# Kernel tuning notes

Hardware: AMD Instinct MI355X
Metric: run time of the kernel (lower is better)

## Reference

```python
import jax, jax.numpy as jnp
import numpy as np

N = 50000      # nodes
E = 800000     # edges (avg degree 16)
H = 128        # hidden_dim
F_IN = 128     # node_in_dim
EPS = 1e-8     # torch cosine_similarity eps
ALPHA = 0.3


def _xavier(k, shape):
    fan_out, fan_in = shape
    lim = float(np.sqrt(6.0 / (fan_in + fan_out)))
    return jax.random.uniform(k, shape, minval=-lim, maxval=lim, dtype=jnp.float32)


PARAM_SHAPES = [
    ("w_lq", (H, 1)), ("w_lf", (H, F_IN)),
    ("wq0", (H, 1)), ("wq1", (H, H)), ("wq2", (H, H)),
    ("wx0", (H, F_IN)), ("wx1", (H, H)), ("wx2", (H, H)),
    ("wf0", (H, H)), ("wf1", (H, H)), ("wf2", (H, H)),
    ("m1_w1", (H, H)), ("m1_w2", (H, H)),
    ("m2_w1", (1, H)), ("m2_w2", (1, 1)),
]
BIAS_OF = {"w_lq": "b_lq", "w_lf": "b_lf", "wq0": "bq0", "wq1": "bq1", "wq2": "bq2",
           "wx0": "bx0", "wx1": "bx1", "wx2": "bx2", "wf0": "bf0", "wf1": "bf1",
           "wf2": "bf2", "m1_w1": "m1_b1", "m1_w2": "m1_b2", "m2_w1": "m2_b1", "m2_w2": "m2_b2"}


def setup_inputs() -> dict:
    key = jax.random.key(0)
    ks = jax.random.split(key, 3 + len(PARAM_SHAPES))
    inp = {
        "q": 42,
        "feats": jax.random.normal(ks[0], (N, F_IN), dtype=jnp.float32),
        "edge_index": jax.random.randint(ks[1], (2, E), 0, N, dtype=jnp.int64),
        "neg_edge_index": jax.random.randint(ks[2], (2, E), 0, N, dtype=jnp.int64),
    }
    for i, (name, shape) in enumerate(PARAM_SHAPES):
        inp[name] = _xavier(ks[3 + i], shape)
        inp[BIAS_OF[name]] = jnp.zeros((shape[0],), jnp.float32)
    return inp


def _forward(q, feats, edge_index, neg_edge_index,
             w_lq, b_lq, w_lf, b_lf,
             wq0, bq0, wq1, bq1, wq2, bq2,
             wx0, bx0, wx1, bx1, wx2, bx2,
             wf0, bf0, wf1, bf1, wf2, bf2,
             m1_w1, m1_b1, m1_w2, m1_b2,
             m2_w1, m2_b1, m2_w2, m2_b2):
    n = feats.shape[0]
    src, dst = edge_index[0], edge_index[1]

    # GCN symmetric normalization with self-loops (edge_weight = 1)
    deg = jax.ops.segment_sum(jnp.ones(src.shape[0], feats.dtype), dst, num_segments=n) + 1.0
    dis = deg ** -0.5
    norm_e = dis[src] * dis[dst]        # per-edge norm
    inv_deg = 1.0 / deg                 # self-loop norm d^-1/2 * d^-1/2

    def lin(x, W, b):
        return x @ W.T + b

    def gcn(x, W, b):
        xw = x @ W.T                                                      # [n,H]
        agg = jax.ops.segment_sum(xw[src] * norm_e[:, None], dst, num_segments=n)
        return agg + xw * inv_deg[:, None] + b

    querys = jnp.zeros((n, 1), feats.dtype).at[q, 0].set(1.0)
    querys_ = lin(querys, w_lq, b_lq)
    feats_ = lin(feats, w_lf, b_lf)

    # layer 0
    hq = jax.nn.relu(gcn(querys, wq0, bq0))
    h = jax.nn.relu(gcn(feats, wx0, bx0))
    hf = jax.nn.relu(hq + h + gcn(querys_ + feats_, wf0, bf0))
    # middle layer (num_layers - 2 == 1 iteration, eval mode: dropout identity)
    hq = jax.nn.relu(gcn(hq, wq1, bq1))
    h = jax.nn.relu(gcn(h, wx1, bx1))
    hf = jax.nn.relu(hq + h + gcn(hf, wf1, bf1))
    # final layer (no relu)
    hq = gcn(hq, wq2, bq2)
    h = gcn(h, wx2, bx2)
    hf = hq + h + gcn(hf, wf2, bf2)

    x = lin(jax.nn.relu(lin(hf, m1_w1, m1_b1)), m1_w2, m1_b2)  # mlp1

    # ---- decode (attack_type != 'proposed') ----
    q_emb = x[q]
    qn = jnp.maximum(jnp.linalg.norm(q_emb), EPS)

    def cos_q(v):  # cosine similarity of rows of v with q_emb (torch eps semantics)
        vn = jnp.maximum(jnp.linalg.norm(v, axis=-1), EPS)
        return (v @ q_emb) / (vn * qn)

    # reconstruct loss: BCE-with-logits on cosine edge scores
    pos_s = cos_q((x[src] + x[dst]) * 0.5)
    neg_s = cos_q((x[neg_edge_index[0]] + x[neg_edge_index[1]]) * 0.5)
    loss_recon = jnp.mean(jax.nn.softplus(-pos_s)) + jnp.mean(jax.nn.softplus(neg_s))

    sim_xq = cos_q(x)                                            # [n]
    sim_xx = lin(jax.nn.relu(lin(x, m2_w1, m2_b1)), m2_w2, m2_b2)[:, 0]  # mlp2
    sim = ((1.0 - ALPHA) * sim_xq + ALPHA * sim_xx) * 2.0
    return jax.nn.sigmoid(sim), loss_recon


def reference(q, feats, edge_index, neg_edge_index,
              w_lq, b_lq, w_lf, b_lf,
              wq0, bq0, wq1, bq1, wq2, bq2,
              wx0, bx0, wx1, bx1, wx2, bx2,
              wf0, bf0, wf1, bf1, wf2, bf2,
              m1_w1, m1_b1, m1_w2, m1_b2,
              m2_w1, m2_b1, m2_w2, m2_b2):
    return _forward(q, feats, edge_index, neg_edge_index,
                    w_lq, b_lq, w_lf, b_lf,
                    wq0, bq0, wq1, bq1, wq2, bq2,
                    wx0, bx0, wx1, bx1, wx2, bx2,
                    wf0, bf0, wf1, bf1, wf2, bf2,
                    m1_w1, m1_b1, m1_w2, m1_b2,
                    m2_w1, m2_b1, m2_w2, m2_b2)
```

## Files before the change

### kernel.cpp

```cpp
#include <hip/hip_runtime.h>
#include <math.h>

#define N_NODES 50000
#define N_EDGES 800000
#define EPSV 1e-8f
#define ALPHA 0.3f

typedef __attribute__((ext_vector_type(8))) unsigned short ushort8;
typedef __attribute__((ext_vector_type(8))) short short8;
typedef __attribute__((ext_vector_type(4))) float floatx4;

__device__ inline float b2f(unsigned short u) {
    union { unsigned i; float f; } c; c.i = ((unsigned)u) << 16; return c.f;
}
__device__ inline unsigned short f2b(float f) {
    union { float f; unsigned i; } c; c.f = f;
    return (unsigned short)((c.i + 0x7FFFu + ((c.i >> 16) & 1u)) >> 16);
}


__global__ __launch_bounds__(256) void k_count(const int* __restrict__ ei,
                                               int* __restrict__ cnt) {
    int e = blockIdx.x * 256 + threadIdx.x;
    if (e < N_EDGES) atomicAdd(&cnt[ei[N_EDGES + e]], 1);
}

__global__ __launch_bounds__(256) void k_invdis(const int* __restrict__ cnt,
                                                float* __restrict__ dis,
                                                float* __restrict__ inv) {
    int i = blockIdx.x * 256 + threadIdx.x;
    if (i < N_NODES) {
        float d = (float)cnt[i] + 1.0f;
        dis[i] = 1.0f / sqrtf(d);
        inv[i] = 1.0f / d;
    }
}

__global__ __launch_bounds__(256) void k_scan_partial(const int* __restrict__ cnt,
                                                      int* __restrict__ partial) {
    int b = blockIdx.x, t = threadIdx.x;
    int base = b * 1024 + t * 4;
    int s = 0;
#pragma unroll
    for (int j = 0; j < 4; ++j) {
        int idx = base + j;
        if (idx < N_NODES) s += cnt[idx];
    }
#pragma unroll
    for (int m = 1; m < 64; m <<= 1) s += __shfl_xor(s, m, 64);
    __shared__ int sh[4];
    if ((t & 63) == 0) sh[t >> 6] = s;
    __syncthreads();
    if (t == 0) partial[b] = sh[0] + sh[1] + sh[2] + sh[3];
}

__global__ void k_scan_mid(int* __restrict__ partial, int* __restrict__ rowptr) {
    int l = threadIdx.x;
    const int NP = (N_NODES + 1023) / 1024;
    int v = (l < NP) ? partial[l] : 0;
    int vin = v;
#pragma unroll
    for (int off = 1; off < 64; off <<= 1) {
        int u = __shfl_up(v, off, 64);
        if (l >= off) v += u;
    }
    if (l < NP) partial[l] = v - vin;
    if (l == NP - 1) rowptr[N_NODES] = v;
}

__global__ __launch_bounds__(256) void k_scan_final(const int* __restrict__ cnt,
                                                    const int* __restrict__ partial,
                                                    int* __restrict__ rowptr) {
    int b = blockIdx.x, t = threadIdx.x;
    int base = b * 1024 + t * 4;
    int c[4];
    int s = 0;
#pragma unroll
    for (int j = 0; j < 4; ++j) {
        int idx = base + j;
        c[j] = (idx < N_NODES) ? cnt[idx] : 0;
        s += c[j];
    }
    __shared__ int sh[256];
    sh[t] = s;
    __syncthreads();
    for (int off = 1; off < 256; off <<= 1) {
        int v = 0;
        if (t >= off) v = sh[t - off];
        __syncthreads();
        sh[t] += v;
        __syncthreads();
    }
    int texcl = sh[t] - s;
    int pre = partial[b] + texcl;
#pragma unroll
    for (int j = 0; j < 4; ++j) {
        int idx = base + j;
        if (idx < N_NODES) rowptr[idx] = pre;
        pre += c[j];
    }
}

__global__ __launch_bounds__(256) void k_fill(const int* __restrict__ ei,
                                              const int* __restrict__ rowptr,
                                              int* __restrict__ cursor,
                                              int* __restrict__ col) {
    int e = blockIdx.x * 256 + threadIdx.x;
    if (e < N_EDGES) {
        int d = ei[N_EDGES + e];
        int pos = rowptr[d] + atomicAdd(&cursor[d], 1);
        col[pos] = ei[e];
    }
}

__global__ __launch_bounds__(256) void k_t(const int* __restrict__ ei,
                                           const int* __restrict__ qp,
                                           const float* __restrict__ dis,
                                           const float* __restrict__ inv,
                                           float* __restrict__ t) {
    int e = blockIdx.x * 256 + threadIdx.x;
    int q = *qp;
    if (e == 0) atomicAdd(&t[q], inv[q]);
    if (e < N_EDGES && ei[e] == q) {
        int d = ei[N_EDGES + e];
        atomicAdd(&t[d], dis[q] * dis[d]);
    }
}

__global__ __launch_bounds__(256) void k_cast(const float* __restrict__ in,
                                              unsigned short* __restrict__ out, int n8) {
    int id = blockIdx.x * 256 + threadIdx.x;
    if (id >= n8) return;
    const float4 a = *(const float4*)(in + id * 8);
    const float4 b = *(const float4*)(in + id * 8 + 4);
    ushort8 o;
    o[0] = f2b(a.x); o[1] = f2b(a.y); o[2] = f2b(a.z); o[3] = f2b(a.w);
    o[4] = f2b(b.x); o[5] = f2b(b.y); o[6] = f2b(b.z); o[7] = f2b(b.w);
    *(ushort8*)(out + id * 8) = o;
}


template <int RELU, int NADD, int HASB2, int WF32>
__global__ __launch_bounds__(256) void k_gemm(
    const unsigned short* __restrict__ A, int As,
    const float* __restrict__ W,
    const float* __restrict__ bias, const float* __restrict__ bias2,
    const unsigned short* __restrict__ add1, int a1s,
    const unsigned short* __restrict__ add2, int a2s,
    unsigned short* __restrict__ outh, int ohs,
    float* __restrict__ outf, int ofs, int nrows) {
    __shared__ unsigned short Al[128 * 128];
    __shared__ unsigned short Wl[128 * 128];
    const int tid = threadIdx.x;
    const int row0 = blockIdx.x * 128;
    const int t4 = tid >> 4, c16 = tid & 15;

#pragma unroll
    for (int it = 0; it < 8; ++it) {
        int r = it * 16 + t4;
        int gr = row0 + r; if (gr > nrows - 1) gr = nrows - 1;
        ushort8 v = *(const ushort8*)(A + (size_t)gr * As + c16 * 8);
        int boff = (c16 * 16) ^ ((r & 7) << 4);
        *(ushort8*)((char*)Al + r * 256 + boff) = v;
    }
#pragma unroll
    for (int it = 0; it < 8; ++it) {
        int c = it * 16 + t4;
        const float* wp = W + c * 128 + c16 * 8;
        float4 w0 = *(const float4*)wp;
        float4 w1 = *(const float4*)(wp + 4);
        ushort8 v;
        v[0] = f2b(w0.x); v[1] = f2b(w0.y); v[2] = f2b(w0.z); v[3] = f2b(w0.w);
        v[4] = f2b(w1.x); v[5] = f2b(w1.y); v[6] = f2b(w1.z); v[7] = f2b(w1.w);
        int boff = (c16 * 16) ^ ((c & 7) << 4);
        *(ushort8*)((char*)Wl + c * 256 + boff) = v;
    }
    __syncthreads();

    const int wv = tid >> 6, l = tid & 63;
    const int lr = l & 15, lg = l >> 4;
    const int sx = (lr & 7) << 4;

    floatx4 acc[8][2];
#pragma unroll
    for (int i = 0; i < 8; ++i)
#pragma unroll
        for (int j = 0; j < 2; ++j) acc[i][j] = (floatx4){0.f, 0.f, 0.f, 0.f};

#pragma unroll
    for (int ks = 0; ks < 4; ++ks) {
        int ko = (ks * 64 + lg * 16) ^ sx;
        short8 bfr[2];
#pragma unroll
        for (int ct = 0; ct < 2; ++ct) {
            int c = wv * 32 + ct * 16 + lr;
            bfr[ct] = *(const short8*)((char*)Wl + c * 256 + ko);
        }
#pragma unroll
        for (int rt = 0; rt < 8; ++rt) {
            int r = rt * 16 + lr;
            short8 af = *(const short8*)((char*)Al + r * 256 + ko);
            acc[rt][0] = __builtin_amdgcn_mfma_f32_16x16x32_bf16(af, bfr[0], acc[rt][0], 0, 0, 0);
            acc[rt][1] = __builtin_amdgcn_mfma_f32_16x16x32_bf16(af, bfr[1], acc[rt][1], 0, 0, 0);
        }
    }

#pragma unroll
    for (int ct = 0; ct < 2; ++ct) {
        int colc = wv * 32 + ct * 16 + lr;
        float bv = bias[colc];
        if (HASB2) bv += bias2[colc];
#pragma unroll
        for (int rt = 0; rt < 8; ++rt) {
            int rbase = row0 + rt * 16 + lg * 4;
#pragma unroll
            for (int reg = 0; reg < 4; ++reg) {
                int r = rbase + reg;
                if (r >= nrows) continue;
                float v = acc[rt][ct][reg] + bv;
                if (NADD >= 1) v += b2f(add1[(size_t)r * a1s + colc]);
                if (NADD >= 2) v += b2f(add2[(size_t)r * a2s + colc]);
                if (RELU) v = fmaxf(v, 0.f);
                outh[(size_t)r * ohs + colc] = f2b(v);
                if (WF32) outf[(size_t)r * ofs + colc] = v;
            }
        }
    }
}


__global__ void k_agg(const int* __restrict__ rowptr, const int* __restrict__ col,
                      const float* __restrict__ dis, const float* __restrict__ inv,
                      const unsigned short* __restrict__ in, int ins, int incb,
                      unsigned short* __restrict__ out, int outs, int outcb) {
    int i = blockIdx.x;
    int cb = blockIdx.y * 128;
    int l = threadIdx.x;
    int g = l >> 4, li = l & 15;
    int r0 = rowptr[i], r1 = rowptr[i + 1];
    float acc[8] = {0.f, 0.f, 0.f, 0.f, 0.f, 0.f, 0.f, 0.f};
    for (int base = r0; base < r1; base += 4) {
        int e = base + g;
        float w = 0.f;
        int s = i;
        if (e < r1) { s = col[e]; w = dis[s]; }
        ushort8 v = *(const ushort8*)(in + (size_t)s * ins + incb + cb + li * 8);
#pragma unroll
        for (int j = 0; j < 8; ++j) acc[j] = fmaf(w, b2f(v[j]), acc[j]);
    }
#pragma unroll
    for (int j = 0; j < 8; ++j) {
        acc[j] += __shfl_xor(acc[j], 16, 64);
        acc[j] += __shfl_xor(acc[j], 32, 64);
    }
    if (g == 0) {
        ushort8 sv = *(const ushort8*)(in + (size_t)i * ins + incb + cb + li * 8);
        float di = dis[i], iv = inv[i];
        ushort8 o;
#pragma unroll
        for (int j = 0; j < 8; ++j) o[j] = f2b(fmaf(di, acc[j], iv * b2f(sv[j])));
        *(ushort8*)(out + (size_t)i * outs + outcb + cb + li * 8) = o;
    }
}

__global__ __launch_bounds__(256) void k_hq0(const float* __restrict__ t,
                                             const float* __restrict__ wq0,
                                             const float* __restrict__ bq0,
                                             unsigned short* __restrict__ B1h) {
    int gidx = blockIdx.x * 256 + threadIdx.x;
    int i = gidx >> 7, j = gidx & 127;
    B1h[(size_t)i * 384 + j] = f2b(fmaxf(fmaf(t[i], wq0[j], bq0[j]), 0.f));
}

__global__ void k_addwlq(const int* __restrict__ qp, const float* __restrict__ w_lq,
                         unsigned short* __restrict__ z0h) {
    int j = threadIdx.x;
    int q = *qp;
    z0h[(size_t)q * 128 + j] = f2b(b2f(z0h[(size_t)q * 128 + j]) + w_lq[j]);
}


__global__ void k_qemb(const int* __restrict__ qp, const float* __restrict__ xf,
                       float* __restrict__ qe) {
    int j = threadIdx.x;
    int q = *qp;
    float v = xf[(size_t)q * 128 + j];
    qe[j] = v;
    float s = v * v;
#pragma unroll
    for (int m = 1; m < 64; m <<= 1) s += __shfl_xor(s, m, 64);
    __shared__ float sh[2];
    if ((j & 63) == 0) sh[j >> 6] = s;
    __syncthreads();
    if (j == 0) qe[128] = fmaxf(sqrtf(sh[0] + sh[1]), EPSV);
}

__global__ __launch_bounds__(256) void k_node(const float* __restrict__ xf,
                                              const float* __restrict__ qe,
                                              const float* __restrict__ m2w1,
                                              const float* __restrict__ m2b1,
                                              const float* __restrict__ m2w2,
                                              const float* __restrict__ m2b2,
                                              float* __restrict__ out,
                                              float* __restrict__ a,
                                              float* __restrict__ n2) {
    int node = blockIdx.x * 4 + (threadIdx.x >> 6);
    int lane = threadIdx.x & 63;
    const float2 xv = *(const float2*)(xf + (size_t)node * 128 + 2 * lane);
    const float2 qv = *(const float2*)(qe + 2 * lane);
    const float2 wv = *(const float2*)(m2w1 + 2 * lane);
    float dq = xv.x * qv.x + xv.y * qv.y;
    float dx = xv.x * xv.x + xv.y * xv.y;
    float dw = xv.x * wv.x + xv.y * wv.y;
#pragma unroll
    for (int m = 1; m < 64; m <<= 1) {
        dq += __shfl_xor(dq, m, 64);
        dx += __shfl_xor(dx, m, 64);
        dw += __shfl_xor(dw, m, 64);
    }
    if (lane == 0) {
        float qn = qe[128];
        float vn = fmaxf(sqrtf(dx), EPSV);
        float simq = dq / (vn * qn);
        float l1 = dw + m2b1[0];
        float s2 = fmaxf(l1, 0.f) * m2w2[0] + m2b2[0];
        float sim = ((1.f - ALPHA) * simq + ALPHA * s2) * 2.f;
        out[node] = 1.f / (1.f + expf(-sim));
        a[node] = dq;
        n2[node] = dx;
    }
}

__global__ __launch_bounds__(256) void k_loss(const int* __restrict__ ei,
                                              const int* __restrict__ nei,
                                              const unsigned short* __restrict__ xh,
                                              const float* __restrict__ a,
                                              const float* __restrict__ n2,
                                              const float* __restrict__ qe,
                                              float* __restrict__ lossout) {
    int l = threadIdx.x & 63, wvi = threadIdx.x >> 6;
    int g = l >> 4, li = l & 15;
    float qn = qe[128];
    float local = 0.f;
    const int tot = 2 * N_EDGES;
    const int stride = gridDim.x * 16;
    for (int e = blockIdx.x * 16 + wvi * 4 + g; e < tot; e += stride) {
        const int* Ep = (e < N_EDGES) ? ei : nei;
        int eo = (e < N_EDGES) ? e : e - N_EDGES;
        int s = Ep[eo], d = Ep[eo + N_EDGES];
        ushort8 va = *(const ushort8*)(xh + (size_t)s * 128 + li * 8);
        ushort8 vb = *(const ushort8*)(xh + (size_t)d * 128 + li * 8);
        float dsd = 0.f;
#pragma unroll
        for (int j = 0; j < 8; ++j) dsd = fmaf(b2f(va[j]), b2f(vb[j]), dsd);
        dsd += __shfl_xor(dsd, 1, 64);
        dsd += __shfl_xor(dsd, 2, 64);
        dsd += __shfl_xor(dsd, 4, 64);
        dsd += __shfl_xor(dsd, 8, 64);
        if (li == 0) {
            float nv = 0.25f * (n2[s] + n2[d] + 2.f * dsd);
            float vn = fmaxf(sqrtf(fmaxf(nv, 0.f)), EPSV);
            float num = 0.5f * (a[s] + a[d]);
            float cs = num / (vn * qn);
            float sg = (e < N_EDGES) ? -cs : cs;
            local += log1pf(expf(sg));
        }
    }
    local += __shfl_xor(local, 16, 64);
    local += __shfl_xor(local, 32, 64);
    __shared__ float sh[4];
    if (l == 0) sh[wvi] = local;
    __syncthreads();
    if (threadIdx.x == 0)
        atomicAdd(lossout, (sh[0] + sh[1] + sh[2] + sh[3]) * (1.f / N_EDGES));
}


extern "C" void kernel_launch(void* const* d_in, const int* in_sizes, int n_in,
                              void* d_out, int out_size, void* d_ws, size_t ws_size,
                              hipStream_t stream) {
    const int* qp = (const int*)d_in[0];
    const float* feats = (const float*)d_in[1];
    const int* ei = (const int*)d_in[2];
    const int* nei = (const int*)d_in[3];
    const float *w_lq = (const float*)d_in[4], *b_lq = (const float*)d_in[5];
    const float *w_lf = (const float*)d_in[6], *b_lf = (const float*)d_in[7];
    const float *wq0 = (const float*)d_in[8], *bq0 = (const float*)d_in[9];
    const float *wq1 = (const float*)d_in[10], *bq1 = (const float*)d_in[11];
    const float *wq2 = (const float*)d_in[12], *bq2 = (const float*)d_in[13];
    const float *wx0 = (const float*)d_in[14], *bx0 = (const float*)d_in[15];
    const float *wx1 = (const float*)d_in[16], *bx1 = (const float*)d_in[17];
    const float *wx2 = (const float*)d_in[18], *bx2 = (const float*)d_in[19];
    const float *wf0 = (const float*)d_in[20], *bf0 = (const float*)d_in[21];
    const float *wf1 = (const float*)d_in[22], *bf1 = (const float*)d_in[23];
    const float *wf2 = (const float*)d_in[24], *bf2 = (const float*)d_in[25];
    const float *m1w1 = (const float*)d_in[26], *m1b1 = (const float*)d_in[27];
    const float *m1w2 = (const float*)d_in[28], *m1b2 = (const float*)d_in[29];
    const float *m2w1 = (const float*)d_in[30], *m2b1 = (const float*)d_in[31];
    const float *m2w2 = (const float*)d_in[32], *m2b2 = (const float*)d_in[33];
    float* out = (float*)d_out;

    char* p = (char*)d_ws;
    auto alloc = [&](size_t b) -> char* {
        char* r = p;
        p += (b + 255) & ~(size_t)255;
        return r;
    };
    float* dis = (float*)alloc(N_NODES * 4);
    float* inv = (float*)alloc(N_NODES * 4);
    float* t = (float*)alloc(N_NODES * 4);
    float* qe = (float*)alloc(129 * 4);
    float* a = (float*)alloc(N_NODES * 4);
    float* n2 = (float*)alloc(N_NODES * 4);
    int* cnt = (int*)alloc(N_NODES * 4);
    int* cursor = (int*)alloc(N_NODES * 4);
    int* rowptr = (int*)alloc((N_NODES + 1) * 4);
    int* partial = (int*)alloc(64 * 4);
    int* col = (int*)alloc(N_EDGES * 4);
    unsigned short* featsh = (unsigned short*)alloc((size_t)N_NODES * 128 * 2);
    unsigned short* z0h = (unsigned short*)alloc((size_t)N_NODES * 128 * 2);
    unsigned short* B1h = (unsigned short*)alloc((size_t)N_NODES * 384 * 2);
    unsigned short* B2h = (unsigned short*)alloc((size_t)N_NODES * 384 * 2);
    unsigned short* xh = (unsigned short*)alloc((size_t)N_NODES * 128 * 2);
    float* xf = (float*)alloc((size_t)N_NODES * 128 * 4);

    const int EB = (N_EDGES + 255) / 256;
    const int NB = (N_NODES + 255) / 256;
    const int NP = (N_NODES + 1023) / 1024;
    const int GB = (N_NODES + 127) / 128;

    hipMemsetAsync(cnt, 0, N_NODES * 4, stream);
    hipMemsetAsync(cursor, 0, N_NODES * 4, stream);
    hipMemsetAsync(t, 0, N_NODES * 4, stream);
    hipMemsetAsync(out + N_NODES, 0, 4, stream);

    k_count<<<EB, 256, 0, stream>>>(ei, cnt);
    k_invdis<<<NB, 256, 0, stream>>>(cnt, dis, inv);
    k_scan_partial<<<NP, 256, 0, stream>>>(cnt, partial);
    k_scan_mid<<<1, 64, 0, stream>>>(partial, rowptr);
    k_scan_final<<<NP, 256, 0, stream>>>(cnt, partial, rowptr);
    k_fill<<<EB, 256, 0, stream>>>(ei, rowptr, cursor, col);
    k_t<<<EB, 256, 0, stream>>>(ei, qp, dis, inv, t);
    k_cast<<<(N_NODES * 128 / 8 + 255) / 256, 256, 0, stream>>>(feats, featsh,
                                                                N_NODES * 128 / 8);

    k_gemm<0, 0, 1, 0><<<GB, 256, 0, stream>>>(featsh, 128, w_lf, b_lf, b_lq,
                                               nullptr, 0, nullptr, 0,
                                               z0h, 128, nullptr, 0, N_NODES);
    k_addwlq<<<1, 128, 0, stream>>>(qp, w_lq, z0h);

    k_hq0<<<(N_NODES * 128) / 256, 256, 0, stream>>>(t, wq0, bq0, B1h);
    k_agg<<<dim3(N_NODES, 1), 64, 0, stream>>>(rowptr, col, dis, inv, featsh, 128, 0,
                                               B2h, 384, 128);
    k_agg<<<dim3(N_NODES, 1), 64, 0, stream>>>(rowptr, col, dis, inv, z0h, 128, 0,
                                               B2h, 384, 256);
    k_gemm<1, 0, 0, 0><<<GB, 256, 0, stream>>>(B2h + 128, 384, wx0, bx0, nullptr,
                                               nullptr, 0, nullptr, 0,
                                               B1h + 128, 384, nullptr, 0, N_NODES);
    k_gemm<1, 2, 0, 0><<<GB, 256, 0, stream>>>(B2h + 256, 384, wf0, bf0, nullptr,
                                               B1h + 0, 384, B1h + 128, 384,
                                               B1h + 256, 384, nullptr, 0, N_NODES);

    k_agg<<<dim3(N_NODES, 3), 64, 0, stream>>>(rowptr, col, dis, inv, B1h, 384, 0,
                                               B2h, 384, 0);
    k_gemm<1, 0, 0, 0><<<GB, 256, 0, stream>>>(B2h + 0, 384, wq1, bq1, nullptr,
                                               nullptr, 0, nullptr, 0,
                                               B1h + 0, 384, nullptr, 0, N_NODES);
    k_gemm<1, 0, 0, 0><<<GB, 256, 0, stream>>>(B2h + 128, 384, wx1, bx1, nullptr,
                                               nullptr, 0, nullptr, 0,
                                               B1h + 128, 384, nullptr, 0, N_NODES);
    k_gemm<1, 2, 0, 0><<<GB, 256, 0, stream>>>(B2h + 256, 384, wf1, bf1, nullptr,
                                               B1h + 0, 384, B1h + 128, 384,
                                               B1h + 256, 384, nullptr, 0, N_NODES);

    k_agg<<<dim3(N_NODES, 3), 64, 0, stream>>>(rowptr, col, dis, inv, B1h, 384, 0,
                                               B2h, 384, 0);
    k_gemm<0, 0, 0, 0><<<GB, 256, 0, stream>>>(B2h + 0, 384, wq2, bq2, nullptr,
                                               nullptr, 0, nullptr, 0,
                                               B1h + 0, 384, nullptr, 0, N_NODES);
    k_gemm<0, 0, 0, 0><<<GB, 256, 0, stream>>>(B2h + 128, 384, wx2, bx2, nullptr,
                                               nullptr, 0, nullptr, 0,
                                               B1h + 128, 384, nullptr, 0, N_NODES);
    k_gemm<0, 2, 0, 0><<<GB, 256, 0, stream>>>(B2h + 256, 384, wf2, bf2, nullptr,
                                               B1h + 0, 384, B1h + 128, 384,
                                               B1h + 256, 384, nullptr, 0, N_NODES);

    k_gemm<1, 0, 0, 0><<<GB, 256, 0, stream>>>(B1h + 256, 384, m1w1, m1b1, nullptr,
                                               nullptr, 0, nullptr, 0,
                                               B2h + 0, 384, nullptr, 0, N_NODES);
    k_gemm<0, 0, 0, 1><<<GB, 256, 0, stream>>>(B2h + 0, 384, m1w2, m1b2, nullptr,
                                               nullptr, 0, nullptr, 0,
                                               xh, 128, xf, 128, N_NODES);

    k_qemb<<<1, 128, 0, stream>>>(qp, xf, qe);
    k_node<<<N_NODES / 4, 256, 0, stream>>>(xf, qe, m2w1, m2b1, m2w2, m2b2, out, a, n2);
    k_loss<<<4096, 256, 0, stream>>>(ei, nei, xh, a, n2, qe, out + N_NODES);
}
```

Baseline: 734.3 us.

## Pre-cast weights to bf16, load GEMM tiles via global_load_lds, batch agg rows, fp16 loss dot

All eleven 128x128 weight matrices are now converted to bf16 once by a single batched kernel, so GEMM blocks no longer convert fp32 weights per block. GEMM tiles for A and W are fetched with direct global-to-LDS loads that keep the swizzled layout. The aggregation kernel now packs four nodes per 256-thread block instead of one node per 64-thread block. The final x is stored as fp16 and the loss kernel uses packed fdot2 products, which changes numerics from bf16 to fp16 for that path.

Result: no change. 737.4 us (+0.4%).

```diff
diff --git a/kernel.cpp b/kernel.cpp
--- a/kernel.cpp
+++ b/kernel.cpp
@@ -9,6 +9,7 @@
 typedef __attribute__((ext_vector_type(8))) unsigned short ushort8;
 typedef __attribute__((ext_vector_type(8))) short short8;
 typedef __attribute__((ext_vector_type(4))) float floatx4;
+typedef _Float16 half2v __attribute__((ext_vector_type(2)));
 
 __device__ inline float b2f(unsigned short u) {
     union { unsigned i; float f; } c; c.i = ((unsigned)u) << 16; return c.f;
@@ -16,6 +17,9 @@
 __device__ inline unsigned short f2b(float f) {
     union { float f; unsigned i; } c; c.f = f;
     return (unsigned short)((c.i + 0x7FFFu + ((c.i >> 16) & 1u)) >> 16);
+}
+__device__ inline unsigned short f2h(float f) {
+    union { _Float16 h; unsigned short u; } c; c.h = (_Float16)f; return c.u;
 }
 
 
@@ -139,11 +143,24 @@
     *(ushort8*)(out + id * 8) = o;
 }
 
-
-template <int RELU, int NADD, int HASB2, int WF32>
+struct WPack { const float* w[11]; };
+__global__ __launch_bounds__(256) void k_castw(WPack wp, unsigned short* __restrict__ out) {
+    int m = blockIdx.y;
+    int id = blockIdx.x * 256 + threadIdx.x;
+    const float* src = wp.w[m] + id * 8;
+    float4 a = *(const float4*)src;
+    float4 b = *(const float4*)(src + 4);
+    ushort8 o;
+    o[0] = f2b(a.x); o[1] = f2b(a.y); o[2] = f2b(a.z); o[3] = f2b(a.w);
+    o[4] = f2b(b.x); o[5] = f2b(b.y); o[6] = f2b(b.z); o[7] = f2b(b.w);
+    *(ushort8*)(out + m * 16384 + id * 8) = o;
+}
+
+
+template <int RELU, int NADD, int HASB2, int WOUT>
 __global__ __launch_bounds__(256) void k_gemm(
     const unsigned short* __restrict__ A, int As,
-    const float* __restrict__ W,
+    const unsigned short* __restrict__ Wb,
     const float* __restrict__ bias, const float* __restrict__ bias2,
     const unsigned short* __restrict__ add1, int a1s,
     const unsigned short* __restrict__ add2, int a2s,
@@ -153,31 +170,28 @@
     __shared__ unsigned short Wl[128 * 128];
     const int tid = threadIdx.x;
     const int row0 = blockIdx.x * 128;
+    const int wv = tid >> 6;
     const int t4 = tid >> 4, c16 = tid & 15;
 
 #pragma unroll
     for (int it = 0; it < 8; ++it) {
         int r = it * 16 + t4;
         int gr = row0 + r; if (gr > nrows - 1) gr = nrows - 1;
-        ushort8 v = *(const ushort8*)(A + (size_t)gr * As + c16 * 8);
-        int boff = (c16 * 16) ^ ((r & 7) << 4);
-        *(ushort8*)((char*)Al + r * 256 + boff) = v;
-    }
-#pragma unroll
-    for (int it = 0; it < 8; ++it) {
-        int c = it * 16 + t4;
-        const float* wp = W + c * 128 + c16 * 8;
-        float4 w0 = *(const float4*)wp;
-        float4 w1 = *(const float4*)(wp + 4);
-        ushort8 v;
-        v[0] = f2b(w0.x); v[1] = f2b(w0.y); v[2] = f2b(w0.z); v[3] = f2b(w0.w);
-        v[4] = f2b(w1.x); v[5] = f2b(w1.y); v[6] = f2b(w1.z); v[7] = f2b(w1.w);
-        int boff = (c16 * 16) ^ ((c & 7) << 4);
-        *(ushort8*)((char*)Wl + c * 256 + boff) = v;
+        int sw = (c16 * 16) ^ ((r & 7) << 4);
+        const char* srcA = (const char*)(A + (size_t)gr * As) + sw;
+        __builtin_amdgcn_global_load_lds(
+            (const __attribute__((address_space(1))) void*)srcA,
+            (__attribute__((address_space(3))) void*)(Al + it * 2048 + wv * 512),
+            16, 0, 0);
+        const char* srcW = (const char*)(Wb + r * 128) + sw;
+        __builtin_amdgcn_global_load_lds(
+            (const __attribute__((address_space(1))) void*)srcW,
+            (__attribute__((address_space(3))) void*)(Wl + it * 2048 + wv * 512),
+            16, 0, 0);
     }
     __syncthreads();
 
-    const int wv = tid >> 6, l = tid & 63;
+    const int l = tid & 63;
     const int lr = l & 15, lg = l >> 4;
     const int sx = (lr & 7) << 4;
 
@@ -221,21 +235,26 @@
                 if (NADD >= 1) v += b2f(add1[(size_t)r * a1s + colc]);
                 if (NADD >= 2) v += b2f(add2[(size_t)r * a2s + colc]);
                 if (RELU) v = fmaxf(v, 0.f);
-                outh[(size_t)r * ohs + colc] = f2b(v);
-                if (WF32) outf[(size_t)r * ofs + colc] = v;
+                if (WOUT) {
+                    outh[(size_t)r * ohs + colc] = f2h(v);
+                    outf[(size_t)r * ofs + colc] = v;
+                } else {
+                    outh[(size_t)r * ohs + colc] = f2b(v);
+                }
             }
         }
     }
 }
 
 
-__global__ void k_agg(const int* __restrict__ rowptr, const int* __restrict__ col,
-                      const float* __restrict__ dis, const float* __restrict__ inv,
-                      const unsigned short* __restrict__ in, int ins, int incb,
-                      unsigned short* __restrict__ out, int outs, int outcb) {
-    int i = blockIdx.x;
+__global__ __launch_bounds__(256) void k_agg(
+    const int* __restrict__ rowptr, const int* __restrict__ col,
+    const float* __restrict__ dis, const float* __restrict__ inv,
+    const unsigned short* __restrict__ in, int ins,
+    unsigned short* __restrict__ out, int outs, int outcb) {
+    int i = blockIdx.x * 4 + (threadIdx.x >> 6);
     int cb = blockIdx.y * 128;
-    int l = threadIdx.x;
+    int l = threadIdx.x & 63;
     int g = l >> 4, li = l & 15;
     int r0 = rowptr[i], r1 = rowptr[i + 1];
     float acc[8] = {0.f, 0.f, 0.f, 0.f, 0.f, 0.f, 0.f, 0.f};
@@ -244,7 +263,7 @@
         float w = 0.f;
         int s = i;
         if (e < r1) { s = col[e]; w = dis[s]; }
-        ushort8 v = *(const ushort8*)(in + (size_t)s * ins + incb + cb + li * 8);
+        ushort8 v = *(const ushort8*)(in + (size_t)s * ins + cb + li * 8);
 #pragma unroll
         for (int j = 0; j < 8; ++j) acc[j] = fmaf(w, b2f(v[j]), acc[j]);
     }
@@ -254,7 +273,7 @@
         acc[j] += __shfl_xor(acc[j], 32, 64);
     }
     if (g == 0) {
-        ushort8 sv = *(const ushort8*)(in + (size_t)i * ins + incb + cb + li * 8);
+        ushort8 sv = *(const ushort8*)(in + (size_t)i * ins + cb + li * 8);
         float di = dis[i], iv = inv[i];
         ushort8 o;
 #pragma unroll
@@ -348,11 +367,13 @@
         const int* Ep = (e < N_EDGES) ? ei : nei;
         int eo = (e < N_EDGES) ? e : e - N_EDGES;
         int s = Ep[eo], d = Ep[eo + N_EDGES];
-        ushort8 va = *(const ushort8*)(xh + (size_t)s * 128 + li * 8);
-        ushort8 vb = *(const ushort8*)(xh + (size_t)d * 128 + li * 8);
+        union { ushort8 u; half2v h[4]; } va, vb;
+        va.u = *(const ushort8*)(xh + (size_t)s * 128 + li * 8);
+        vb.u = *(const ushort8*)(xh + (size_t)d * 128 + li * 8);
         float dsd = 0.f;
 #pragma unroll
-        for (int j = 0; j < 8; ++j) dsd = fmaf(b2f(va[j]), b2f(vb[j]), dsd);
+        for (int j = 0; j < 4; ++j)
+            dsd = __builtin_amdgcn_fdot2(va.h[j], vb.h[j], dsd, false);
         dsd += __shfl_xor(dsd, 1, 64);
         dsd += __shfl_xor(dsd, 2, 64);
         dsd += __shfl_xor(dsd, 4, 64);
@@ -417,6 +438,7 @@
     int* rowptr = (int*)alloc((N_NODES + 1) * 4);
     int* partial = (int*)alloc(64 * 4);
     int* col = (int*)alloc(N_EDGES * 4);
+    unsigned short* Wb = (unsigned short*)alloc((size_t)11 * 16384 * 2);
     unsigned short* featsh = (unsigned short*)alloc((size_t)N_NODES * 128 * 2);
     unsigned short* z0h = (unsigned short*)alloc((size_t)N_NODES * 128 * 2);
     unsigned short* B1h = (unsigned short*)alloc((size_t)N_NODES * 384 * 2);
@@ -443,52 +465,54 @@
     k_t<<<EB, 256, 0, stream>>>(ei, qp, dis, inv, t);
     k_cast<<<(N_NODES * 128 / 8 + 255) / 256, 256, 0, stream>>>(feats, featsh,
                                                                 N_NODES * 128 / 8);
-
-    k_gemm<0, 0, 1, 0><<<GB, 256, 0, stream>>>(featsh, 128, w_lf, b_lf, b_lq,
+    WPack wp{{w_lf, wx0, wf0, wq1, wx1, wf1, wq2, wx2, wf2, m1w1, m1w2}};
+    k_castw<<<dim3(8, 11), 256, 0, stream>>>(wp, Wb);
+
+    k_gemm<0, 0, 1, 0><<<GB, 256, 0, stream>>>(featsh, 128, Wb + 0 * 16384, b_lf, b_lq,
                                                nullptr, 0, nullptr, 0,
                                                z0h, 128, nullptr, 0, N_NODES);
     k_addwlq<<<1, 128, 0, stream>>>(qp, w_lq, z0h);
 
     k_hq0<<<(N_NODES * 128) / 256, 256, 0, stream>>>(t, wq0, bq0, B1h);
-    k_agg<<<dim3(N_NODES, 1), 64, 0, stream>>>(rowptr, col, dis, inv, featsh, 128, 0,
-                                               B2h, 384, 128);
-    k_agg<<<dim3(N_NODES, 1), 64, 0, stream>>>(rowptr, col, dis, inv, z0h, 128, 0,
-                                               B2h, 384, 256);
-    k_gemm<1, 0, 0, 0><<<GB, 256, 0, stream>>>(B2h + 128, 384, wx0, bx0, nullptr,
+    k_agg<<<dim3(N_NODES / 4, 1), 256, 0, stream>>>(rowptr, col, dis, inv, featsh, 128,
+                                                    B2h, 384, 128);
+    k_agg<<<dim3(N_NODES / 4, 1), 256, 0, stream>>>(rowptr, col, dis, inv, z0h, 128,
+                                                    B2h, 384, 256);
+    k_gemm<1, 0, 0, 0><<<GB, 256, 0, stream>>>(B2h + 128, 384, Wb + 1 * 16384, bx0, nullptr,
                                                nullptr, 0, nullptr, 0,
                                                B1h + 128, 384, nullptr, 0, N_NODES);
-    k_gemm<1, 2, 0, 0><<<GB, 256, 0, stream>>>(B2h + 256, 384, wf0, bf0, nullptr,
+    k_gemm<1, 2, 0, 0><<<GB, 256, 0, stream>>>(B2h + 256, 384, Wb + 2 * 16384, bf0, nullptr,
                                                B1h + 0, 384, B1h + 128, 384,
                                                B1h + 256, 384, nullptr, 0, N_NODES);
 
-    k_agg<<<dim3(N_NODES, 3), 64, 0, stream>>>(rowptr, col, dis, inv, B1h, 384, 0,
-                                               B2h, 384, 0);
-    k_gemm<1, 0, 0, 0><<<GB, 256, 0, stream>>>(B2h + 0, 384, wq1, bq1, nullptr,
+    k_agg<<<dim3(N_NODES / 4, 3), 256, 0, stream>>>(rowptr, col, dis, inv, B1h, 384,
+                                                    B2h, 384, 0);
+    k_gemm<1, 0, 0, 0><<<GB, 256, 0, stream>>>(B2h + 0, 384, Wb + 3 * 16384, bq1, nullptr,
                                                nullptr, 0, nullptr, 0,
                                                B1h + 0, 384, nullptr, 0, N_NODES);
-    k_gemm<1, 0, 0, 0><<<GB, 256, 0, stream>>>(B2h + 128, 384, wx1, bx1, nullptr,
+    k_gemm<1, 0, 0, 0><<<GB, 256, 0, stream>>>(B2h + 128, 384, Wb + 4 * 16384, bx1, nullptr,
                                                nullptr, 0, nullptr, 0,
                                                B1h + 128, 384, nullptr, 0, N_NODES);
-    k_gemm<1, 2, 0, 0><<<GB, 256, 0, stream>>>(B2h + 256, 384, wf1, bf1, nullptr,
+    k_gemm<1, 2, 0, 0><<<GB, 256, 0, stream>>>(B2h + 256, 384, Wb + 5 * 16384, bf1, nullptr,
                                                B1h + 0, 384, B1h + 128, 384,
                                                B1h + 256, 384, nullptr, 0, N_NODES);
 
-    k_agg<<<dim3(N_NODES, 3), 64, 0, stream>>>(rowptr, col, dis, inv, B1h, 384, 0,
-                                               B2h, 384, 0);
-    k_gemm<0, 0, 0, 0><<<GB, 256, 0, stream>>>(B2h + 0, 384, wq2, bq2, nullptr,
+    k_agg<<<dim3(N_NODES / 4, 3), 256, 0, stream>>>(rowptr, col, dis, inv, B1h, 384,
+                                                    B2h, 384, 0);
+    k_gemm<0, 0, 0, 0><<<GB, 256, 0, stream>>>(B2h + 0, 384, Wb + 6 * 16384, bq2, nullptr,
                                                nullptr, 0, nullptr, 0,
                                                B1h + 0, 384, nullptr, 0, N_NODES);
-    k_gemm<0, 0, 0, 0><<<GB, 256, 0, stream>>>(B2h + 128, 384, wx2, bx2, nullptr,
+    k_gemm<0, 0, 0, 0><<<GB, 256, 0, stream>>>(B2h + 128, 384, Wb + 7 * 16384, bx2, nullptr,
                                                nullptr, 0, nullptr, 0,
                                                B1h + 128, 384, nullptr, 0, N_NODES);
-    k_gemm<0, 2, 0, 0><<<GB, 256, 0, stream>>>(B2h + 256, 384, wf2, bf2, nullptr,
+    k_gemm<0, 2, 0, 0><<<GB, 256, 0, stream>>>(B2h + 256, 384, Wb + 8 * 16384, bf2, nullptr,
                                                B1h + 0, 384, B1h + 128, 384,
                                                B1h + 256, 384, nullptr, 0, N_NODES);
 
-    k_gemm<1, 0, 0, 0><<<GB, 256, 0, stream>>>(B1h + 256, 384, m1w1, m1b1, nullptr,
+    k_gemm<1, 0, 0, 0><<<GB, 256, 0, stream>>>(B1h + 256, 384, Wb + 9 * 16384, m1b1, nullptr,
                                                nullptr, 0, nullptr, 0,
                                                B2h + 0, 384, nullptr, 0, N_NODES);
-    k_gemm<0, 0, 0, 1><<<GB, 256, 0, stream>>>(B2h + 0, 384, m1w2, m1b2, nullptr,
+    k_gemm<0, 0, 0, 1><<<GB, 256, 0, stream>>>(B2h + 0, 384, Wb + 10 * 16384, m1b2, nullptr,
                                                nullptr, 0, nullptr, 0,
                                                xh, 128, xf, 128, N_NODES);
 
```
